# Optimization experiments

Measured on AMD Instinct MI355X. Metric: run time of the kernel, lower is better.

The kernel has to match this reference:

```python
import jax, jax.numpy as jnp
import numpy as np

# Module hyperparams (match init_kwargs)
INITIAL_NOISE = 64
NOISE = 16
HIDDEN = 64
MLP = 128
T = 128
BATCH = 4096


def _lipswish(x):
    # torch.nn.LipSwish from the sde-gan codebase: 0.909 * x * sigmoid(x)
    return 0.909 * jax.nn.silu(x)


def _mlp(x, w0, b0, w1, b1, w2, b2, tanh):
    # MLP(in, out, mlp_size, num_layers=2): Linear+LipSwish, Linear+LipSwish, Linear[, Tanh]
    h = _lipswish(x @ w0 + b0)
    h = _lipswish(h @ w1 + b1)
    o = h @ w2 + b2
    return jnp.tanh(o) if tanh else o


def setup_inputs() -> dict:
    key = jax.random.key(0)
    ks = jax.random.split(key, 20)
    s = 0.1  # weight scale to avoid tanh saturation
    inp = {
        "ts": jnp.arange(T, dtype=jnp.float32),
        "batch_size": BATCH,
        "init_noise": jax.random.normal(ks[0], (BATCH, INITIAL_NOISE), jnp.float32),
        "dW": jax.random.normal(ks[1], (T - 1, BATCH, NOISE), jnp.float32),
        # initial MLP: initial_noise_size -> hidden (no tanh)
        "iw0": jax.random.normal(ks[2], (INITIAL_NOISE, MLP), jnp.float32) * s,
        "ib0": jax.random.normal(ks[3], (MLP,), jnp.float32) * s,
        "iw1": jax.random.normal(ks[4], (MLP, MLP), jnp.float32) * s,
        "ib1": jax.random.normal(ks[5], (MLP,), jnp.float32) * s,
        "iw2": jax.random.normal(ks[6], (MLP, HIDDEN), jnp.float32) * s,
        "ib2": jax.random.normal(ks[7], (HIDDEN,), jnp.float32) * s,
        # diffusion MLP: 1+hidden -> hidden*noise (tanh)
        "gw0": jax.random.normal(ks[8], (1 + HIDDEN, MLP), jnp.float32) * s,
        "gb0": jax.random.normal(ks[9], (MLP,), jnp.float32) * s,
        "gw1": jax.random.normal(ks[10], (MLP, MLP), jnp.float32) * s,
        "gb1": jax.random.normal(ks[11], (MLP,), jnp.float32) * s,
        "gw2": jax.random.normal(ks[12], (MLP, HIDDEN * NOISE), jnp.float32) * s,
        "gb2": jax.random.normal(ks[13], (HIDDEN * NOISE,), jnp.float32) * s,
        # readout: hidden -> 1
        "rw": jax.random.normal(ks[14], (HIDDEN, 1), jnp.float32) * s,
        "rb": jax.random.normal(ks[15], (1,), jnp.float32) * s,
    }
    return inp


def reference(ts, batch_size, init_noise, dW,
              iw0, ib0, iw1, ib1, iw2, ib2,
              gw0, gb0, gw1, gb1, gw2, gb2,
              rw, rb):
    B = init_noise.shape[0]

    def g_fn(t, x):
        # f_and_g: tx = cat([t.expand(B,1), x], dim=1); diffusion -> (B, hidden, noise)
        tx = jnp.concatenate([jnp.full((B, 1), t, x.dtype), x], axis=1)
        g = _mlp(tx, gw0, gb0, gw1, gb1, gw2, gb2, tanh=True)
        return g.reshape(B, HIDDEN, NOISE)

    x0 = _mlp(init_noise, iw0, ib0, iw1, ib1, iw2, ib2, tanh=False)  # (B, hidden)

    dt = ts[1:] - ts[:-1]                       # (T-1,)
    dW_s = dW * jnp.sqrt(dt)[:, None, None]     # Brownian increments ~ N(0, dt)

    g0 = g_fn(ts[0], x0)

    # Reversible Heun (drift is identically zero in GeneratorFunc.f_and_g):
    #   zhat_{n+1} = 2 z_n - zhat_n + ghat_n dW_n
    #   g_{n+1}    = g(t_{n+1}, zhat_{n+1})
    #   z_{n+1}    = z_n + 0.5 (ghat_n + g_{n+1}) dW_n
    def step(carry, inp):
        z, zhat, ghat = carry
        t1, dWn = inp
        zhat_new = 2.0 * z - zhat + jnp.einsum('bhn,bn->bh', ghat, dWn)
        g_new = g_fn(t1, zhat_new)
        z_new = z + jnp.einsum('bhn,bn->bh', 0.5 * (ghat + g_new), dWn)
        return (z_new, zhat_new, g_new), z_new

    (_, _, _), zs = jax.lax.scan(step, (x0, x0, g0), (ts[1:], dW_s))
    xs = jnp.concatenate([x0[None], zs], axis=0)        # (T, B, hidden)
    xs = jnp.transpose(xs, (1, 0, 2))                   # (B, T, hidden)
    ys = xs @ rw + rb                                   # (B, T, 1)
    ts_b = jnp.broadcast_to(ts[None, :, None], (B, ts.shape[0], 1))
    # linear_interpolation_coeffs with no NaNs is the identity on the data
    return jnp.concatenate([ts_b, ys], axis=2)          # (B, T, 2)
```

## Files before the change

### kernel.cpp

```cpp
#include <hip/hip_runtime.h>

typedef unsigned short u16;
typedef _Float16 f16;
typedef __attribute__((ext_vector_type(8))) _Float16 f16x8;
typedef __attribute__((ext_vector_type(4))) float f32x4;

#define B_TOT 4096
#define T_STEPS 128
#define SMEM_BYTES 113024
#define LSCALE 2048.f
#define LINV   4.8828125e-4f

__device__ __forceinline__ u16 f2h(float x) {
  union { f16 h; u16 u; } v; v.h = (f16)x; return v.u;
}
__device__ __forceinline__ float h2f(u16 b) {
  union { u16 u; f16 h; } v; v.u = b; return (float)v.h;
}
__device__ __forceinline__ void split2(float x, u16& h, u16& l) {
  h = f2h(x);
  float r = x - h2f(h);
  l = f2h(r * LSCALE);
}
__device__ __forceinline__ float fastrcp(float x) {
  return __builtin_amdgcn_rcpf(x);
}
__device__ __forceinline__ float lsw(float u) {
  return 0.909f * u * fastrcp(1.f + __expf(-u));
}
__device__ __forceinline__ float tanh_fast(float u) {
  return 1.f - 2.f * fastrcp(1.f + __expf(2.f * u));
}
__device__ __forceinline__ f32x4 mmh(f16x8 a, f16x8 b, f32x4 c) {
  return __builtin_amdgcn_mfma_f32_16x16x32_f16(a, b, c, 0, 0, 0);
}
__device__ __forceinline__ f16x8 ldfrag(const u16* p) { return *(const f16x8*)p; }

__global__ void frag_w2(const float* __restrict__ W, int KS, int ldW, int rowOff,
                        u16* __restrict__ dh, u16* __restrict__ dl, int nElems) {
  int i = blockIdx.x * blockDim.x + threadIdx.x;
  if (i >= nElems) return;
  int e = i & 7, lane = (i >> 3) & 63, rest = i >> 9;
  int ks = rest % KS, nt = rest / KS;
  int row = rowOff + ks * 32 + ((lane >> 4) * 8) + e;
  int col = nt * 16 + (lane & 15);
  float w = W[row * ldW + col];
  u16 h, l; split2(w, h, l);
  dh[i] = h; dl[i] = l;
}

__global__ __launch_bounds__(512, 1) void sde_gen(
    const float* __restrict__ ts, const float* __restrict__ init_noise,
    const float* __restrict__ dW,
    const float* __restrict__ ib0, const float* __restrict__ ib1, const float* __restrict__ ib2,
    const float* __restrict__ gw0, const float* __restrict__ gb0,
    const float* __restrict__ gb1, const float* __restrict__ gb2,
    const float* __restrict__ rw, const float* __restrict__ rb,
    const u16* __restrict__ fiw0h, const u16* __restrict__ fiw0l,
    const u16* __restrict__ fiw1h, const u16* __restrict__ fiw1l,
    const u16* __restrict__ fiw2h, const u16* __restrict__ fiw2l,
    const u16* __restrict__ fgw0h, const u16* __restrict__ fgw0l,
    const u16* __restrict__ fgw1h, const u16* __restrict__ fgw1l,
    const u16* __restrict__ fgw2h, const u16* __restrict__ fgw2l,
    float* __restrict__ out) {
  extern __shared__ char smem[];
  u16*   s_w1h  = (u16*)(smem);
  u16*   s_w1l  = (u16*)(smem + 32768);
  u16*   s_ax   = (u16*)(smem + 65536);
  u16*   s_ah0  = (u16*)(smem + 70144);
  u16*   s_ah1  = (u16*)(smem + 78848);
  float* s_z    = (float*)(smem + 87552);
  float* s_zh   = (float*)(smem + 91648);
  float* s_v    = (float*)(smem + 95744);
  float* s_w    = (float*)(smem + 100096);
  float* s_dw   = (float*)(smem + 104448);
  float* s_ts   = (float*)(smem + 106624);
  float* s_gb0  = (float*)(smem + 107136);
  float* s_w0r0 = (float*)(smem + 107648);
  float* s_gb1  = (float*)(smem + 108160);
  float* s_gb2  = (float*)(smem + 108672);
  float* s_rw   = (float*)(smem + 112768);
#define AX(L,r,c)   s_ax [((L)*16+(r))*72 +(c)]
#define AH0(L,r,c)  s_ah0[((L)*16+(r))*136+(c)]
#define AH1(L,r,c)  s_ah1[((L)*16+(r))*136+(c)]
#define ZV(r,c)  s_z [(r)*64+(c)]
#define ZH(r,c)  s_zh[(r)*64+(c)]
#define SV(r,c)  s_v [(r)*68+(c)]
#define SW(r,c)  s_w [(r)*68+(c)]
#define SDW(b,r,c) s_dw[((b)*16+(r))*17+(c)]

  const int tid = threadIdx.x;
  const int wv = tid >> 6;
  const int lane = tid & 63;
  const int l15 = lane & 15, lg = lane >> 4;
  const int R = blockIdx.x * 16;
  const int jrot = blockIdx.x & 7;

  for (int i = tid; i < 128; i += 512) {
    s_ts[i] = ts[i]; s_gb0[i] = gb0[i]; s_gb1[i] = gb1[i]; s_w0r0[i] = gw0[i];
  }
  for (int i = tid; i < 1024; i += 512) s_gb2[i] = gb2[i];
  if (tid < 64) s_rw[tid] = rw[tid];
  for (int i = tid; i < 2048; i += 512) {
    ((f16x8*)s_w1h)[i] = ((const f16x8*)fgw1h)[i];
    ((f16x8*)s_w1l)[i] = ((const f16x8*)fgw1l)[i];
  }
  for (int i = tid; i < 16 * 64; i += 512) {
    int r = i >> 6, k = i & 63;
    float x = init_noise[(R + r) * 64 + k];
    u16 h, l; split2(x, h, l);
    AX(0,r,k) = h; AX(1,r,k) = l;
  }
  if (tid < 256) {
    float sdt = sqrtf(ts[1] - ts[0]);
    int r = tid >> 4, nn = tid & 15;
    SDW(0, r, nn) = dW[(0 * B_TOT + R + r) * 16 + nn] * sdt;
    SDW(1, r, nn) = 0.f;
  }
  __syncthreads();

  {
    f32x4 aA = {0,0,0,0}, aB = {0,0,0,0};
#pragma unroll
    for (int ks = 0; ks < 2; ++ks) {
      f16x8 xh = *(const f16x8*)&AX(0, l15, ks*32 + lg*8);
      f16x8 xl = *(const f16x8*)&AX(1, l15, ks*32 + lg*8);
      int off = ((wv * 2 + ks) * 64 + lane) * 8;
      f16x8 bh = ldfrag(fiw0h + off), bl = ldfrag(fiw0l + off);
      aA = mmh(xh, bh, aA);
      aB = mmh(xh, bl, mmh(xl, bh, aB));
    }
#pragma unroll
    for (int reg = 0; reg < 4; ++reg) {
      int r = lg * 4 + reg, c = wv * 16 + l15;
      float act = lsw((aA[reg] + aB[reg] * LINV) + ib0[c]);
      u16 h, l; split2(act, h, l);
      AH0(0,r,c) = h; AH0(1,r,c) = l;
    }
  }
  __syncthreads();
  {
    f32x4 aA = {0,0,0,0}, aB = {0,0,0,0};
#pragma unroll
    for (int ks = 0; ks < 4; ++ks) {
      f16x8 xh = *(const f16x8*)&AH0(0, l15, ks*32 + lg*8);
      f16x8 xl = *(const f16x8*)&AH0(1, l15, ks*32 + lg*8);
      int off = ((wv * 4 + ks) * 64 + lane) * 8;
      f16x8 bh = ldfrag(fiw1h + off), bl = ldfrag(fiw1l + off);
      aA = mmh(xh, bh, aA);
      aB = mmh(xh, bl, mmh(xl, bh, aB));
    }
#pragma unroll
    for (int reg = 0; reg < 4; ++reg) {
      int r = lg * 4 + reg, c = wv * 16 + l15;
      float act = lsw((aA[reg] + aB[reg] * LINV) + ib1[c]);
      u16 h, l; split2(act, h, l);
      AH1(0,r,c) = h; AH1(1,r,c) = l;
    }
  }
  __syncthreads();
  if (wv < 4) {
    f32x4 aA = {0,0,0,0}, aB = {0,0,0,0};
#pragma unroll
    for (int ks = 0; ks < 4; ++ks) {
      f16x8 xh = *(const f16x8*)&AH1(0, l15, ks*32 + lg*8);
      f16x8 xl = *(const f16x8*)&AH1(1, l15, ks*32 + lg*8);
      int off = ((wv * 4 + ks) * 64 + lane) * 8;
      f16x8 bh = ldfrag(fiw2h + off), bl = ldfrag(fiw2l + off);
      aA = mmh(xh, bh, aA);
      aB = mmh(xh, bl, mmh(xl, bh, aB));
    }
#pragma unroll
    for (int reg = 0; reg < 4; ++reg) {
      int r = lg * 4 + reg, c = wv * 16 + l15;
      float x0 = (aA[reg] + aB[reg] * LINV) + ib2[c];
      ZV(r,c) = x0; ZH(r,c) = x0;
      u16 h, l; split2(x0, h, l);
      AX(0,r,c) = h; AX(1,r,c) = l;
    }
  }
  __syncthreads();

  const float rbv = rb[0];

#define L3_COMPUTE(WH, WL, NT)                                                  \
  {                                                                             \
    f32x4 aA = {0,0,0,0}, aB = {0,0,0,0};                                       \
    _Pragma("unroll")                                                           \
    for (int ks = 0; ks < 4; ++ks) {                                            \
      aA = mmh(WH[ks], bfh[ks], aA);                                            \
      aB = mmh(WH[ks], bfl[ks], mmh(WL[ks], bfh[ks], aB));                      \
    }                                                                           \
    float pw = 0.f, pv = 0.f;                                                   \
    _Pragma("unroll")                                                           \
    for (int reg = 0; reg < 4; ++reg) {                                         \
      int c = (NT) * 16 + lg * 4 + reg;                                         \
      float g = tanh_fast((aA[reg] + aB[reg] * LINV) + s_gb2[c]);               \
      pw += g * dw0v[reg];                                                      \
      pv += g * dw1v[reg];                                                      \
    }                                                                           \
    pw += __shfl_xor(pw, 16); pw += __shfl_xor(pw, 32);                         \
    pv += __shfl_xor(pv, 16); pv += __shfl_xor(pv, 32);                         \
    if (lane < 16) { SW(lane, (NT)) = pw; SV(lane, (NT)) = pv; }                \
  }

#define L3_PREFETCH(WH, WL, NT)                                                 \
  {                                                                             \
    _Pragma("unroll")                                                           \
    for (int ks = 0; ks < 4; ++ks) {                                            \
      int off = (((NT) * 4 + ks) * 64 + lane) * 8;                              \
      WH[ks] = ldfrag(fgw2h + off);                                             \
      WL[ks] = ldfrag(fgw2l + off);                                             \
    }                                                                           \
  }

  for (int n = 0; n < T_STEPS; ++n) {
    if (n > 0) {
#pragma unroll
      for (int i = 0; i < 2; ++i) {
        int r = wv * 2 + i, h = lane;
        float z = ZV(r,h), zh = ZH(r,h), v = SV(r,h);
        float zhn = 2.f * z - zh + v;
        ZH(r,h) = zhn;
        u16 hh, ll; split2(zhn, hh, ll);
        AX(0,r,h) = hh; AX(1,r,h) = ll;
        ZV(r,h) = z + 0.5f * v;
      }
      if (n < T_STEPS - 1 && tid < 256) {
        float sdt = sqrtf(s_ts[n + 1] - s_ts[n]);
        int r = tid >> 4, nn = tid & 15;
        SDW(n & 1, r, nn) = dW[(n * B_TOT + R + r) * 16 + nn] * sdt;
      }
      __syncthreads();
    }
    const float tval = s_ts[n];
    {
      f32x4 aA = {0,0,0,0}, aB = {0,0,0,0};
#pragma unroll
      for (int ks = 0; ks < 2; ++ks) {
        f16x8 xh = *(const f16x8*)&AX(0, l15, ks*32 + lg*8);
        f16x8 xl = *(const f16x8*)&AX(1, l15, ks*32 + lg*8);
        int off = ((wv * 2 + ks) * 64 + lane) * 8;
        f16x8 bh = ldfrag(fgw0h + off);
        f16x8 bl = ldfrag(fgw0l + off);
        aA = mmh(xh, bh, aA);
        aB = mmh(xh, bl, mmh(xl, bh, aB));
      }
#pragma unroll
      for (int reg = 0; reg < 4; ++reg) {
        int r = lg * 4 + reg, c = wv * 16 + l15;
        float act = lsw((aA[reg] + aB[reg] * LINV) + s_gb0[c] + tval * s_w0r0[c]);
        u16 h, l; split2(act, h, l);
        AH0(0,r,c) = h; AH0(1,r,c) = l;
      }
    }
    __syncthreads();
    f16x8 whA[4], wlA[4], whB[4], wlB[4];
    {
      L3_PREFETCH(whA, wlA, wv * 8 + jrot);
      f32x4 aA = {0,0,0,0}, aB = {0,0,0,0};
#pragma unroll
      for (int ks = 0; ks < 4; ++ks) {
        f16x8 xh = *(const f16x8*)&AH0(0, l15, ks*32 + lg*8);
        f16x8 xl = *(const f16x8*)&AH0(1, l15, ks*32 + lg*8);
        int off = ((wv * 4 + ks) * 64 + lane) * 8;
        f16x8 bh = *(const f16x8*)&s_w1h[off];
        f16x8 bl = *(const f16x8*)&s_w1l[off];
        aA = mmh(xh, bh, aA);
        aB = mmh(xh, bl, mmh(xl, bh, aB));
      }
#pragma unroll
      for (int reg = 0; reg < 4; ++reg) {
        int r = lg * 4 + reg, c = wv * 16 + l15;
        float act = lsw((aA[reg] + aB[reg] * LINV) + s_gb1[c]);
        u16 h, l; split2(act, h, l);
        AH1(0,r,c) = h; AH1(1,r,c) = l;
      }
    }
    __syncthreads();
    float dw0v[4], dw1v[4];
#pragma unroll
    for (int reg = 0; reg < 4; ++reg) {
      dw0v[reg] = SDW((n - 1) & 1, l15, lg * 4 + reg);
      dw1v[reg] = SDW(n & 1,       l15, lg * 4 + reg);
    }
    f16x8 bfh[4], bfl[4];
#pragma unroll
    for (int ks = 0; ks < 4; ++ks) {
      bfh[ks] = *(const f16x8*)&AH1(0, l15, ks*32 + lg*8);
      bfl[ks] = *(const f16x8*)&AH1(1, l15, ks*32 + lg*8);
    }
#pragma unroll 1
    for (int j = 0; j < 8; j += 2) {
      const int ntA = wv * 8 + ((j + jrot) & 7);
      const int ntB = wv * 8 + ((j + 1 + jrot) & 7);
      L3_PREFETCH(whB, wlB, ntB);
      L3_COMPUTE(whA, wlA, ntA);
      if (j < 6) {
        const int ntA2 = wv * 8 + ((j + 2 + jrot) & 7);
        L3_PREFETCH(whA, wlA, ntA2);
      }
      L3_COMPUTE(whB, wlB, ntB);
    }
    __syncthreads();
#pragma unroll
    for (int i = 0; i < 2; ++i) {
      int r = wv * 2 + i, h = lane;
      float z = ZV(r,h);
      if (n > 0) { z += 0.5f * SW(r,h); ZV(r,h) = z; }
      float p = z * s_rw[h];
#pragma unroll
      for (int off = 32; off >= 1; off >>= 1) p += __shfl_xor(p, off);
      if (lane == 0) {
        int o = ((R + r) * T_STEPS + n) * 2;
        out[o] = tval; out[o + 1] = p + rbv;
      }
    }
  }
}

extern "C" void kernel_launch(void* const* d_in, const int* in_sizes, int n_in,
                              void* d_out, int out_size, void* d_ws, size_t ws_size,
                              hipStream_t stream) {
  (void)in_sizes; (void)n_in; (void)out_size; (void)ws_size;
  const float* ts = (const float*)d_in[0];
  const float* init_noise = (const float*)d_in[2];
  const float* dW  = (const float*)d_in[3];
  const float* iw0 = (const float*)d_in[4];
  const float* ib0 = (const float*)d_in[5];
  const float* iw1 = (const float*)d_in[6];
  const float* ib1 = (const float*)d_in[7];
  const float* iw2 = (const float*)d_in[8];
  const float* ib2 = (const float*)d_in[9];
  const float* gw0 = (const float*)d_in[10];
  const float* gb0 = (const float*)d_in[11];
  const float* gw1 = (const float*)d_in[12];
  const float* gb1 = (const float*)d_in[13];
  const float* gw2 = (const float*)d_in[14];
  const float* gb2 = (const float*)d_in[15];
  const float* rw  = (const float*)d_in[16];
  const float* rb  = (const float*)d_in[17];

  u16* ws = (u16*)d_ws;
  const int LO = 188416;
  u16* fiw0h = ws + 0;      u16* fiw0l = ws + LO + 0;
  u16* fiw1h = ws + 8192;   u16* fiw1l = ws + LO + 8192;
  u16* fiw2h = ws + 24576;  u16* fiw2l = ws + LO + 24576;
  u16* fgw0h = ws + 32768;  u16* fgw0l = ws + LO + 32768;
  u16* fgw1h = ws + 40960;  u16* fgw1l = ws + LO + 40960;
  u16* fgw2h = ws + 57344;  u16* fgw2l = ws + LO + 57344;

  frag_w2<<<32,  256, 0, stream>>>(iw0, 2, 128, 0, fiw0h, fiw0l, 8192);
  frag_w2<<<64,  256, 0, stream>>>(iw1, 4, 128, 0, fiw1h, fiw1l, 16384);
  frag_w2<<<32,  256, 0, stream>>>(iw2, 4, 64,  0, fiw2h, fiw2l, 8192);
  frag_w2<<<32,  256, 0, stream>>>(gw0, 2, 128, 1, fgw0h, fgw0l, 8192);
  frag_w2<<<64,  256, 0, stream>>>(gw1, 4, 128, 0, fgw1h, fgw1l, 16384);
  frag_w2<<<512, 256, 0, stream>>>(gw2, 4, 1024, 0, fgw2h, fgw2l, 131072);

  hipFuncSetAttribute((const void*)sde_gen,
                      hipFuncAttributeMaxDynamicSharedMemorySize, SMEM_BYTES);
  sde_gen<<<256, 512, SMEM_BYTES, stream>>>(
      ts, init_noise, dW, ib0, ib1, ib2, gw0, gb0, gb1, gb2, rw, rb,
      fiw0h, fiw0l, fiw1h, fiw1l, fiw2h, fiw2l,
      fgw0h, fgw0l, fgw1h, fgw1l, fgw2h, fgw2l,
      (float*)d_out);
}
```

Baseline: 875.4 us.

## Merge state update into readout phase, keep layer-0 weights in registers, drop jrot

The z/zhat update and dW prefetch for the next step now run at the end of each time step, inside the readout loop. This removes one separate pass and reuses the z value already loaded. The gw0 fragments are loaded into registers once before the time loop instead of every step. The per-block rotation of layer-3 tile order is dropped, and both A and B fragment sets are prefetched before the layer-1 matmul. The costs are higher register pressure and losing whatever L2 or channel spreading the rotation provided.

```diff
diff --git a/kernel.cpp b/kernel.cpp
--- a/kernel.cpp
+++ b/kernel.cpp
@@ -94,7 +94,6 @@
   const int lane = tid & 63;
   const int l15 = lane & 15, lg = lane >> 4;
   const int R = blockIdx.x * 16;
-  const int jrot = blockIdx.x & 7;
 
   for (int i = tid; i < 128; i += 512) {
     s_ts[i] = ts[i]; s_gb0[i] = gb0[i]; s_gb1[i] = gb1[i]; s_w0r0[i] = gw0[i];
@@ -183,7 +182,15 @@
 
   const float rbv = rb[0];
 
-#define L3_COMPUTE(WH, WL, NT)                                                  \
+  f16x8 g0h[2], g0l[2];
+#pragma unroll
+  for (int ks = 0; ks < 2; ++ks) {
+    int off = ((wv * 2 + ks) * 64 + lane) * 8;
+    g0h[ks] = ldfrag(fgw0h + off);
+    g0l[ks] = ldfrag(fgw0l + off);
+  }
+
+#define L3_COMPUTE(WH, WL, TI)                                                  \
   {                                                                             \
     f32x4 aA = {0,0,0,0}, aB = {0,0,0,0};                                       \
     _Pragma("unroll")                                                           \
@@ -194,45 +201,27 @@
     float pw = 0.f, pv = 0.f;                                                   \
     _Pragma("unroll")                                                           \
     for (int reg = 0; reg < 4; ++reg) {                                         \
-      int c = (NT) * 16 + lg * 4 + reg;                                         \
+      int c = (TI) * 16 + lg * 4 + reg;                                         \
       float g = tanh_fast((aA[reg] + aB[reg] * LINV) + s_gb2[c]);               \
       pw += g * dw0v[reg];                                                      \
       pv += g * dw1v[reg];                                                      \
     }                                                                           \
     pw += __shfl_xor(pw, 16); pw += __shfl_xor(pw, 32);                         \
     pv += __shfl_xor(pv, 16); pv += __shfl_xor(pv, 32);                         \
-    if (lane < 16) { SW(lane, (NT)) = pw; SV(lane, (NT)) = pv; }                \
-  }
-
-#define L3_PREFETCH(WH, WL, NT)                                                 \
+    if (lane < 16) { SW(lane, (TI)) = pw; SV(lane, (TI)) = pv; }                \
+  }
+
+#define L3_PREFETCH(WH, WL, TI)                                                 \
   {                                                                             \
     _Pragma("unroll")                                                           \
     for (int ks = 0; ks < 4; ++ks) {                                            \
-      int off = (((NT) * 4 + ks) * 64 + lane) * 8;                              \
+      int off = (((TI) * 4 + ks) * 64 + lane) * 8;                              \
       WH[ks] = ldfrag(fgw2h + off);                                             \
       WL[ks] = ldfrag(fgw2l + off);                                             \
     }                                                                           \
   }
 
   for (int n = 0; n < T_STEPS; ++n) {
-    if (n > 0) {
-#pragma unroll
-      for (int i = 0; i < 2; ++i) {
-        int r = wv * 2 + i, h = lane;
-        float z = ZV(r,h), zh = ZH(r,h), v = SV(r,h);
-        float zhn = 2.f * z - zh + v;
-        ZH(r,h) = zhn;
-        u16 hh, ll; split2(zhn, hh, ll);
-        AX(0,r,h) = hh; AX(1,r,h) = ll;
-        ZV(r,h) = z + 0.5f * v;
-      }
-      if (n < T_STEPS - 1 && tid < 256) {
-        float sdt = sqrtf(s_ts[n + 1] - s_ts[n]);
-        int r = tid >> 4, nn = tid & 15;
-        SDW(n & 1, r, nn) = dW[(n * B_TOT + R + r) * 16 + nn] * sdt;
-      }
-      __syncthreads();
-    }
     const float tval = s_ts[n];
     {
       f32x4 aA = {0,0,0,0}, aB = {0,0,0,0};
@@ -240,11 +229,8 @@
       for (int ks = 0; ks < 2; ++ks) {
         f16x8 xh = *(const f16x8*)&AX(0, l15, ks*32 + lg*8);
         f16x8 xl = *(const f16x8*)&AX(1, l15, ks*32 + lg*8);
-        int off = ((wv * 2 + ks) * 64 + lane) * 8;
-        f16x8 bh = ldfrag(fgw0h + off);
-        f16x8 bl = ldfrag(fgw0l + off);
-        aA = mmh(xh, bh, aA);
-        aB = mmh(xh, bl, mmh(xl, bh, aB));
+        aA = mmh(xh, g0h[ks], aA);
+        aB = mmh(xh, g0l[ks], mmh(xl, g0h[ks], aB));
       }
 #pragma unroll
       for (int reg = 0; reg < 4; ++reg) {
@@ -257,7 +243,8 @@
     __syncthreads();
     f16x8 whA[4], wlA[4], whB[4], wlB[4];
     {
-      L3_PREFETCH(whA, wlA, wv * 8 + jrot);
+      L3_PREFETCH(whA, wlA, wv * 8 + 0);
+      L3_PREFETCH(whB, wlB, wv * 8 + 1);
       f32x4 aA = {0,0,0,0}, aB = {0,0,0,0};
 #pragma unroll
       for (int ks = 0; ks < 4; ++ks) {
@@ -292,22 +279,17 @@
     }
 #pragma unroll 1
     for (int j = 0; j < 8; j += 2) {
-      const int ntA = wv * 8 + ((j + jrot) & 7);
-      const int ntB = wv * 8 + ((j + 1 + jrot) & 7);
-      L3_PREFETCH(whB, wlB, ntB);
-      L3_COMPUTE(whA, wlA, ntA);
-      if (j < 6) {
-        const int ntA2 = wv * 8 + ((j + 2 + jrot) & 7);
-        L3_PREFETCH(whA, wlA, ntA2);
-      }
-      L3_COMPUTE(whB, wlB, ntB);
+      L3_COMPUTE(whA, wlA, wv * 8 + j);
+      if (j < 6) L3_PREFETCH(whA, wlA, wv * 8 + j + 2);
+      L3_COMPUTE(whB, wlB, wv * 8 + j + 1);
+      if (j < 6) L3_PREFETCH(whB, wlB, wv * 8 + j + 3);
     }
     __syncthreads();
 #pragma unroll
     for (int i = 0; i < 2; ++i) {
       int r = wv * 2 + i, h = lane;
       float z = ZV(r,h);
-      if (n > 0) { z += 0.5f * SW(r,h); ZV(r,h) = z; }
+      if (n > 0) z += 0.5f * SW(r,h);
       float p = z * s_rw[h];
 #pragma unroll
       for (int off = 32; off >= 1; off >>= 1) p += __shfl_xor(p, off);
@@ -315,7 +297,22 @@
         int o = ((R + r) * T_STEPS + n) * 2;
         out[o] = tval; out[o + 1] = p + rbv;
       }
-    }
+      if (n < T_STEPS - 1) {
+        float pv = SV(r,h);
+        float zh = ZH(r,h);
+        float zhn = 2.f * z - zh + pv;
+        ZH(r,h) = zhn;
+        ZV(r,h) = z + 0.5f * pv;
+        u16 hh, ll; split2(zhn, hh, ll);
+        AX(0,r,h) = hh; AX(1,r,h) = ll;
+      }
+    }
+    if (n < T_STEPS - 2 && tid < 256) {
+      float sdt = sqrtf(s_ts[n + 2] - s_ts[n + 1]);
+      int r = tid >> 4, nn = tid & 15;
+      SDW((n + 1) & 1, r, nn) = dW[((n + 1) * B_TOT + R + r) * 16 + nn] * sdt;
+    }
+    __syncthreads();
   }
 }
 
```

Measured after the change: 889.7 us. Within noise of the previous version (+1.6%).

## Pin gw2 high-half fragments in AGPRs and fully unroll layer-3 loop

Applied to the files above, without the earlier changes.

Loads the high-half fp16 fragments of the diffusion output weight (gw2) once before the time loop and holds them in accumulator registers through an inline-asm constraint. Inside each step only the low-half fragments are streamed, halving per-step weight fetch traffic for layer 3. The layer-3 tile loop is fully unrolled with sched_barriers to keep the prefetch/compute ordering. This adds 128 AGPR-resident vectors, which raises register pressure and may add AGPR-to-VGPR copies if MFMA cannot read the fragments straight from AGPRs.

```diff
diff --git a/kernel.cpp b/kernel.cpp
--- a/kernel.cpp
+++ b/kernel.cpp
@@ -183,34 +183,45 @@
 
   const float rbv = rb[0];
 
-#define L3_COMPUTE(WH, WL, NT)                                                  \
+  f16x8 w2fh[8][4];
+#pragma unroll
+  for (int j = 0; j < 8; ++j)
+#pragma unroll
+    for (int ks = 0; ks < 4; ++ks)
+      w2fh[j][ks] =
+          ldfrag(fgw2h + (((wv * 8 + ((j + jrot) & 7)) * 4 + ks) * 64 + lane) * 8);
+#pragma unroll
+  for (int j = 0; j < 8; ++j)
+#pragma unroll
+    for (int ks = 0; ks < 4; ++ks)
+      asm volatile("" : "+a"(w2fh[j][ks]));
+
+#define L3_COMPUTE_A(J, WL, TI)                                                 \
   {                                                                             \
     f32x4 aA = {0,0,0,0}, aB = {0,0,0,0};                                       \
     _Pragma("unroll")                                                           \
     for (int ks = 0; ks < 4; ++ks) {                                            \
-      aA = mmh(WH[ks], bfh[ks], aA);                                            \
-      aB = mmh(WH[ks], bfl[ks], mmh(WL[ks], bfh[ks], aB));                      \
+      aA = mmh(w2fh[J][ks], bfh[ks], aA);                                       \
+      aB = mmh(w2fh[J][ks], bfl[ks], mmh(WL[ks], bfh[ks], aB));                 \
     }                                                                           \
     float pw = 0.f, pv = 0.f;                                                   \
     _Pragma("unroll")                                                           \
     for (int reg = 0; reg < 4; ++reg) {                                         \
-      int c = (NT) * 16 + lg * 4 + reg;                                         \
+      int c = (TI) * 16 + lg * 4 + reg;                                         \
       float g = tanh_fast((aA[reg] + aB[reg] * LINV) + s_gb2[c]);               \
       pw += g * dw0v[reg];                                                      \
       pv += g * dw1v[reg];                                                      \
     }                                                                           \
     pw += __shfl_xor(pw, 16); pw += __shfl_xor(pw, 32);                         \
     pv += __shfl_xor(pv, 16); pv += __shfl_xor(pv, 32);                         \
-    if (lane < 16) { SW(lane, (NT)) = pw; SV(lane, (NT)) = pv; }                \
-  }
-
-#define L3_PREFETCH(WH, WL, NT)                                                 \
+    if (lane < 16) { SW(lane, (TI)) = pw; SV(lane, (TI)) = pv; }                \
+  }
+
+#define L3_PREFETCH_L(WL, TI)                                                   \
   {                                                                             \
     _Pragma("unroll")                                                           \
     for (int ks = 0; ks < 4; ++ks) {                                            \
-      int off = (((NT) * 4 + ks) * 64 + lane) * 8;                              \
-      WH[ks] = ldfrag(fgw2h + off);                                             \
-      WL[ks] = ldfrag(fgw2l + off);                                             \
+      WL[ks] = ldfrag(fgw2l + (((TI) * 4 + ks) * 64 + lane) * 8);               \
     }                                                                           \
   }
 
@@ -255,9 +266,17 @@
       }
     }
     __syncthreads();
-    f16x8 whA[4], wlA[4], whB[4], wlB[4];
+    f16x8 wlA[4], wlB[4];
+    const int t0 = wv * 8 + jrot;
+    const int t1 = wv * 8 + ((1 + jrot) & 7);
+    const int t2 = wv * 8 + ((2 + jrot) & 7);
+    const int t3 = wv * 8 + ((3 + jrot) & 7);
+    const int t4 = wv * 8 + ((4 + jrot) & 7);
+    const int t5 = wv * 8 + ((5 + jrot) & 7);
+    const int t6 = wv * 8 + ((6 + jrot) & 7);
+    const int t7 = wv * 8 + ((7 + jrot) & 7);
     {
-      L3_PREFETCH(whA, wlA, wv * 8 + jrot);
+      L3_PREFETCH_L(wlA, t0);
       f32x4 aA = {0,0,0,0}, aB = {0,0,0,0};
 #pragma unroll
       for (int ks = 0; ks < 4; ++ks) {
@@ -290,18 +309,21 @@
       bfh[ks] = *(const f16x8*)&AH1(0, l15, ks*32 + lg*8);
       bfl[ks] = *(const f16x8*)&AH1(1, l15, ks*32 + lg*8);
     }
-#pragma unroll 1
-    for (int j = 0; j < 8; j += 2) {
-      const int ntA = wv * 8 + ((j + jrot) & 7);
-      const int ntB = wv * 8 + ((j + 1 + jrot) & 7);
-      L3_PREFETCH(whB, wlB, ntB);
-      L3_COMPUTE(whA, wlA, ntA);
-      if (j < 6) {
-        const int ntA2 = wv * 8 + ((j + 2 + jrot) & 7);
-        L3_PREFETCH(whA, wlA, ntA2);
-      }
-      L3_COMPUTE(whB, wlB, ntB);
-    }
+    L3_PREFETCH_L(wlB, t1);  L3_COMPUTE_A(0, wlA, t0);
+    __builtin_amdgcn_sched_barrier(0);
+    L3_PREFETCH_L(wlA, t2);  L3_COMPUTE_A(1, wlB, t1);
+    __builtin_amdgcn_sched_barrier(0);
+    L3_PREFETCH_L(wlB, t3);  L3_COMPUTE_A(2, wlA, t2);
+    __builtin_amdgcn_sched_barrier(0);
+    L3_PREFETCH_L(wlA, t4);  L3_COMPUTE_A(3, wlB, t3);
+    __builtin_amdgcn_sched_barrier(0);
+    L3_PREFETCH_L(wlB, t5);  L3_COMPUTE_A(4, wlA, t4);
+    __builtin_amdgcn_sched_barrier(0);
+    L3_PREFETCH_L(wlA, t6);  L3_COMPUTE_A(5, wlB, t5);
+    __builtin_amdgcn_sched_barrier(0);
+    L3_PREFETCH_L(wlB, t7);  L3_COMPUTE_A(6, wlA, t6);
+    __builtin_amdgcn_sched_barrier(0);
+    L3_COMPUTE_A(7, wlB, t7);
     __syncthreads();
 #pragma unroll
     for (int i = 0; i < 2; ++i) {
```

New measurement: 2.867 ms. 227% more time.
